# Kernel optimization log

Hardware: AMD Instinct MI355X
Metric: run time of the kernel (lower is better)

The kernel has to match this reference:

```python
import jax, jax.numpy as jnp
import numpy as np

HEADS = 4
DIM_HEAD = 64
SCALE = 8.0
EPS = 1e-5  # fp32 branch of the original LayerNorm


def setup_inputs() -> dict:
    key = jax.random.key(0)
    k1, k2, k3 = jax.random.split(key, 3)
    B, C, F, H, W = 2, 256, 4, 32, 32
    inner = HEADS * DIM_HEAD  # 256
    x = jax.random.normal(k1, (B, C, F, H, W), dtype=jnp.float32)
    gamma = jnp.ones((1, C, 1, 1, 1), dtype=jnp.float32)
    w_qkv = jax.random.normal(k2, (3 * inner, C), dtype=jnp.float32) * 0.05
    w_out = jax.random.normal(k3, (C, inner), dtype=jnp.float32) * 0.05
    return {"x": x, "gamma": gamma, "w_qkv": w_qkv, "w_out": w_out}


def _l2norm(t):
    return t / jnp.sqrt(jnp.sum(t * t, axis=-1, keepdims=True) + 1e-12)


def reference(x, gamma, w_qkv, w_out):
    B, C, F, H, W = x.shape
    N = F * H * W
    inner = HEADS * DIM_HEAD
    residual = x

    # channel LayerNorm (biased variance over dim=1)
    mean = jnp.mean(x, axis=1, keepdims=True)
    var = jnp.mean((x - mean) ** 2, axis=1, keepdims=True)
    xn = (x - mean) / jnp.sqrt(var + EPS) * gamma

    # 1x1x1 conv == channel matmul; flatten spatial dims to sequence
    xn_flat = xn.reshape(B, C, N)                      # [B, C, N]
    qkv = jnp.einsum('oc,bcn->bon', w_qkv, xn_flat)    # [B, 3*inner, N]
    qkv = qkv.reshape(B, 3, HEADS, DIM_HEAD, N)        # chunk then split heads
    qkv = jnp.transpose(qkv, (1, 0, 2, 4, 3))          # [3, B, h, N, d]
    q, k, v = qkv[0], qkv[1], qkv[2]

    q = _l2norm(q)
    k = _l2norm(k)

    sim = jnp.einsum('bhid,bhjd->bhij', q, k) * SCALE  # [B, h, N, N]
    attn = jax.nn.softmax(sim, axis=-1)
    out = jnp.einsum('bhij,bhjd->bhid', attn, v)       # [B, h, N, d]

    # 'b h n d -> b (h d) n' then 1x1x1 out conv
    out = jnp.transpose(out, (0, 1, 3, 2)).reshape(B, inner, N)
    out = jnp.einsum('oi,bin->bon', w_out, out).reshape(B, C, F, H, W)
    return out + residual
```

## Files before the change

kernel.cpp:

```cpp
#include <hip/hip_runtime.h>

#define BATCH 2
#define CCH   256
#define NSEQ  4096
#define NH    4
#define DH    64
#define INNER 256

typedef __attribute__((ext_vector_type(8))) __bf16 bf16x8;
typedef __attribute__((ext_vector_type(4))) float f32x4;
typedef __attribute__((ext_vector_type(8))) unsigned short u16x8;
typedef __attribute__((ext_vector_type(4))) unsigned short u16x4;

#define GLD16(gsrc, ldst)                                                     \
  __builtin_amdgcn_global_load_lds(                                           \
      (const __attribute__((address_space(1))) unsigned int*)(const void*)(gsrc), \
      (__attribute__((address_space(3))) unsigned int*)(void*)(ldst), 16, 0, 0)

static __device__ __forceinline__ unsigned short f2bfr(float f) {
  union { float f; unsigned u; } v; v.f = f;
  return (unsigned short)((v.u + 0x8000u) >> 16);
}
static __device__ __forceinline__ unsigned pack2(float f0, float f1) {
  union { float f; unsigned u; } a, b; a.f = f0; b.f = f1;
  return __builtin_amdgcn_perm(b.u + 0x8000u, a.u + 0x8000u, 0x07060302u);
}
static __device__ __forceinline__ float bf2f(unsigned short u) {
  union { unsigned u; float f; } v; v.u = ((unsigned)u) << 16;
  return v.f;
}
static __device__ __forceinline__ bf16x8 ldb(const unsigned short* p) {
  return *(const bf16x8*)p;
}
static __device__ __forceinline__ f32x4 mm(bf16x8 a, bf16x8 b, f32x4 c) {
  return __builtin_amdgcn_mfma_f32_16x16x32_bf16(a, b, c, 0, 0, 0);
}

__global__ __launch_bounds__(256) void k_lncvt(const float* __restrict__ x,
                                               const float* __restrict__ gamma,
                                               unsigned short* __restrict__ xn,
                                               const float* __restrict__ wq,
                                               const float* __restrict__ wo,
                                               unsigned short* __restrict__ wqb,
                                               unsigned short* __restrict__ wob) {
  int blk = blockIdx.x;
  if (blk >= 256) {
    int t = (blk - 256) * 256 + threadIdx.x;
    int e = t * 4;
    if (e < 768 * 256) {
      float4 v = *(const float4*)(wq + e);
      u16x4 pk = { f2bfr(v.x), f2bfr(v.y), f2bfr(v.z), f2bfr(v.w) };
      *(u16x4*)(wqb + e) = pk;
    } else {
      int e2 = e - 768 * 256;
      float4 v = *(const float4*)(wo + e2);
      u16x4 pk = { f2bfr(v.x), f2bfr(v.y), f2bfr(v.z), f2bfr(v.w) };
      *(u16x4*)(wob + e2) = pk;
    }
    return;
  }
  int b  = blk >> 7;
  int n0 = (blk & 127) * 32;
  int t  = threadIdx.x;
  int nl = t & 31;
  int cg = t >> 5;
  int n  = n0 + nl;
  const float* xp = x + ((size_t)(b * CCH + cg * 32)) * NSEQ + n;
  float vals[32];
  float s = 0.f, s2 = 0.f;
#pragma unroll
  for (int j = 0; j < 32; j++) {
    float v = xp[(size_t)j * NSEQ];
    vals[j] = v; s += v; s2 += v * v;
  }
  __shared__ float rs[8][32], rs2[8][32];
  rs[cg][nl] = s; rs2[cg][nl] = s2;
  __syncthreads();
  float S = 0.f, S2 = 0.f;
#pragma unroll
  for (int g = 0; g < 8; g++) { S += rs[g][nl]; S2 += rs2[g][nl]; }
  float mean = S * (1.f / 256.f);
  float var  = S2 * (1.f / 256.f) - mean * mean;
  float rstd = rsqrtf(var + 1e-5f);
  unsigned short* dst = xn + ((size_t)b * NSEQ + n) * CCH + cg * 32;
#pragma unroll
  for (int j0 = 0; j0 < 32; j0 += 8) {
    u16x8 pk;
#pragma unroll
    for (int j = 0; j < 8; j++)
      pk[j] = f2bfr((vals[j0 + j] - mean) * rstd * gamma[cg * 32 + j0 + j]);
    *(u16x8*)(dst + j0) = pk;
  }
}

__global__ __launch_bounds__(256) void k_qkv(const unsigned short* __restrict__ wqb,
                                             const unsigned short* __restrict__ xn,
                                             unsigned short* __restrict__ qkv,
                                             unsigned short* __restrict__ qt,
                                             unsigned short* __restrict__ ktb) {
  int n0 = blockIdx.x * 64;
  int oi = blockIdx.y;
  int o0 = oi * 64;
  int b  = blockIdx.z;
  __shared__ unsigned short Al[64 * 128];
  __shared__ unsigned short Bl[64 * 128];
  int t = threadIdx.x;
  int lane = t & 63, w = t >> 6;
  int c = lane & 15, quad = lane >> 4;
  int wm = w >> 1, wn = w & 1;
  f32x4 acc[2][2] = {};
  int lr = lane >> 4;
  int lchk = lane & 15;
  const unsigned short* apg = wqb + (size_t)o0 * CCH;
  const unsigned short* bpg = xn + ((size_t)b * NSEQ + n0) * CCH;
  for (int kt = 0; kt < 2; kt++) {
    if (kt) __syncthreads();
#pragma unroll
    for (int q = 0; q < 4; q++) {
      int r = w * 16 + q * 4 + lr;
      int srcoff = r * CCH + kt * 128 + ((lchk ^ (r & 7)) * 8);
      GLD16(apg + srcoff, Al + (size_t)(w * 16 + q * 4) * 128);
      GLD16(bpg + srcoff, Bl + (size_t)(w * 16 + q * 4) * 128);
    }
    __syncthreads();
#pragma unroll
    for (int ks = 0; ks < 4; ks++) {
      int ra0 = wm * 32 + c, ra1 = ra0 + 16;
      int rb0 = wn * 32 + c, rb1 = rb0 + 16;
      bf16x8 a0 = ldb(&Al[ra0 * 128 + (((ks * 4 + quad) ^ (ra0 & 7)) * 8)]);
      bf16x8 a1 = ldb(&Al[ra1 * 128 + (((ks * 4 + quad) ^ (ra1 & 7)) * 8)]);
      bf16x8 b0 = ldb(&Bl[rb0 * 128 + (((ks * 4 + quad) ^ (rb0 & 7)) * 8)]);
      bf16x8 b1 = ldb(&Bl[rb1 * 128 + (((ks * 4 + quad) ^ (rb1 & 7)) * 8)]);
      acc[0][0] = mm(a0, b0, acc[0][0]);
      acc[0][1] = mm(a0, b1, acc[0][1]);
      acc[1][0] = mm(a1, b0, acc[1][0]);
      acc[1][1] = mm(a1, b1, acc[1][1]);
    }
  }
  if (oi < 8) {
    float* sq = (float*)Al;
    float s0 = 0.f, s1 = 0.f;
#pragma unroll
    for (int i = 0; i < 2; i++)
#pragma unroll
      for (int rr = 0; rr < 4; rr++) {
        s0 += acc[i][0][rr] * acc[i][0][rr];
        s1 += acc[i][1][rr] * acc[i][1][rr];
      }
    s0 += __shfl_xor(s0, 16); s0 += __shfl_xor(s0, 32);
    s1 += __shfl_xor(s1, 16); s1 += __shfl_xor(s1, 32);
    __syncthreads();
    if (quad == 0) {
      sq[wm * 64 + wn * 32 + c]      = s0;
      sq[wm * 64 + wn * 32 + 16 + c] = s1;
    }
    __syncthreads();
    float r0 = rsqrtf(sq[wn * 32 + c]      + sq[64 + wn * 32 + c]      + 1e-12f);
    float r1 = rsqrtf(sq[wn * 32 + 16 + c] + sq[64 + wn * 32 + 16 + c] + 1e-12f);
    if (oi < 4) { r0 *= 11.541560327111707f; r1 *= 11.541560327111707f; }
    int h = oi & 3;
    unsigned short* base = (oi < 4 ? qt : ktb) + ((size_t)(b * NH + h) * NSEQ) * DH;
#pragma unroll
    for (int i = 0; i < 2; i++)
#pragma unroll
      for (int j = 0; j < 2; j++) {
        float rsc = j ? r1 : r0;
        int n = n0 + wn * 32 + j * 16 + c;
        int d = wm * 32 + i * 16 + quad * 4;
        uint2 pk = { pack2(acc[i][j][0] * rsc, acc[i][j][1] * rsc),
                     pack2(acc[i][j][2] * rsc, acc[i][j][3] * rsc) };
        *(uint2*)(base + (size_t)n * DH + d) = pk;
      }
  } else {
#pragma unroll
    for (int i = 0; i < 2; i++)
#pragma unroll
      for (int j = 0; j < 2; j++)
#pragma unroll
        for (int rr = 0; rr < 4; rr++) {
          int o = o0 + wm * 32 + i * 16 + quad * 4 + rr;
          int n = n0 + wn * 32 + j * 16 + c;
          qkv[((size_t)b * 768 + o) * NSEQ + n] = f2bfr(acc[i][j][rr]);
        }
  }
}

__global__ __launch_bounds__(256, 4) void k_attn(
    const unsigned short* __restrict__ qt,
    const unsigned short* __restrict__ ktb,
    const unsigned short* __restrict__ qkv,
    unsigned short* __restrict__ opart,
    float* __restrict__ lpart,
    int S, int kvlen) {
  int i0 = blockIdx.x * 128;
  int h  = blockIdx.y;
  int bz = blockIdx.z;
  int b  = bz / S, s = bz % S;
  __shared__ unsigned short Kl[64 * 64];
  __shared__ unsigned short Vl[64 * 64];
  __shared__ unsigned short Pl[128 * 64];
  int t = threadIdx.x;
  int lane = t & 63, w = t >> 6;
  int c = lane & 15, quad = lane >> 4;

  const unsigned short* qbase = qt  + ((size_t)(b * NH + h) * NSEQ) * DH;
  const unsigned short* kbase = ktb + ((size_t)(b * NH + h) * NSEQ) * DH;
  const unsigned short* vbase = qkv + ((size_t)b * 768 + 512 + h * 64) * NSEQ;

  int rlo = w * 32 + c, rhi = rlo + 16;
  const unsigned short* qlo = qbase + (size_t)(i0 + rlo) * DH + quad * 8;
  const unsigned short* qhi = qlo + 16 * DH;
  bf16x8 qlo0 = ldb(qlo), qlo1 = ldb(qlo + 32);
  bf16x8 qhi0 = ldb(qhi), qhi1 = ldb(qhi + 32);

  u16x8 onesu;
#pragma unroll
  for (int j = 0; j < 8; j++) onesu[j] = 0x3F80;
  bf16x8 ones = *(bf16x8*)&onesu;

  f32x4 acclo[4] = {}, acchi[4] = {};
  f32x4 accllo = {}, acclhi = {};

  int slr = lane >> 3, slc = lane & 7;
  int ssw = (slc ^ slr) * 8;
  const unsigned short* kp = kbase + (size_t)(s * kvlen + w * 16 + slr) * DH + ssw;
  const unsigned short* vp = vbase + (size_t)(w * 16 + slr) * NSEQ + s * kvlen + ssw;
  unsigned short* kl0 = Kl + (w * 16)     * 64;
  unsigned short* kl1 = Kl + (w * 16 + 8) * 64;
  unsigned short* vl0 = Vl + (w * 16)     * 64;
  unsigned short* vl1 = Vl + (w * 16 + 8) * 64;
  int sw0 = (quad ^ (c & 7)) * 8;
  int sw1 = sw0 ^ 32;
  int r7 = rlo & 7;

  for (int it = 0; it < kvlen / 64; it++) {
    GLD16(kp,            kl0);
    GLD16(kp + 8 * DH,   kl1);
    GLD16(vp,            vl0);
    GLD16(vp + 8 * NSEQ, vl1);
    kp += 64 * DH; vp += 64;
    __syncthreads();

#pragma unroll
    for (int jt = 0; jt < 4; jt++) {
      bf16x8 k0 = ldb(&Kl[(jt * 16 + c) * 64 + sw0]);
      bf16x8 k1 = ldb(&Kl[(jt * 16 + c) * 64 + sw1]);
      f32x4 zl = {}; zl = mm(k0, qlo0, zl); zl = mm(k1, qlo1, zl);
      f32x4 zh = {}; zh = mm(k0, qhi0, zh); zh = mm(k1, qhi1, zh);
      int cj = jt * 2 + (quad >> 1);
      int sub = (quad & 1) * 4;
      uint2 pkl = { pack2(exp2f(zl[0]), exp2f(zl[1])),
                    pack2(exp2f(zl[2]), exp2f(zl[3])) };
      *(uint2*)&Pl[rlo * 64 + ((cj ^ r7) * 8) + sub] = pkl;
      uint2 pkh = { pack2(exp2f(zh[0]), exp2f(zh[1])),
                    pack2(exp2f(zh[2]), exp2f(zh[3])) };
      *(uint2*)&Pl[rhi * 64 + ((cj ^ r7) * 8) + sub] = pkh;
    }
    bf16x8 plo0 = ldb(&Pl[rlo * 64 + ((quad ^ r7) * 8)]);
    bf16x8 plo1 = ldb(&Pl[rlo * 64 + (((quad + 4) ^ r7) * 8)]);
    bf16x8 phi0 = ldb(&Pl[rhi * 64 + ((quad ^ r7) * 8)]);
    bf16x8 phi1 = ldb(&Pl[rhi * 64 + (((quad + 4) ^ r7) * 8)]);
#pragma unroll
    for (int dt = 0; dt < 4; dt++) {
      bf16x8 v0 = ldb(&Vl[(dt * 16 + c) * 64 + sw0]);
      bf16x8 v1 = ldb(&Vl[(dt * 16 + c) * 64 + sw1]);
      acclo[dt] = mm(plo0, v0, acclo[dt]);
      acclo[dt] = mm(plo1, v1, acclo[dt]);
      acchi[dt] = mm(phi0, v0, acchi[dt]);
      acchi[dt] = mm(phi1, v1, acchi[dt]);
    }
    accllo = mm(plo0, ones, accllo); accllo = mm(plo1, ones, accllo);
    acclhi = mm(phi0, ones, acclhi); acclhi = mm(phi1, ones, acclhi);
    __syncthreads();
  }

  size_t rb = ((size_t)(b * NH + h) * S + s) * NSEQ + i0 + w * 32;
  if (c == 0) {
#pragma unroll
    for (int rr = 0; rr < 4; rr++) {
      lpart[rb + quad * 4 + rr]      = accllo[rr];
      lpart[rb + 16 + quad * 4 + rr] = acclhi[rr];
    }
  }
#pragma unroll
  for (int rr = 0; rr < 4; rr++)
#pragma unroll
    for (int dt = 0; dt < 4; dt++) {
      opart[(rb + quad * 4 + rr) * 64 + dt * 16 + c]      = f2bfr(acclo[dt][rr]);
      opart[(rb + 16 + quad * 4 + rr) * 64 + dt * 16 + c] = f2bfr(acchi[dt][rr]);
    }
}

__global__ __launch_bounds__(256) void k_out(const unsigned short* __restrict__ wob,
                                             const unsigned short* __restrict__ opart,
                                             const float* __restrict__ lpart,
                                             const float* __restrict__ x,
                                             float* __restrict__ out, int S) {
  int n0 = blockIdx.x * 64;
  int o0 = blockIdx.y * 64;
  int b  = blockIdx.z;
  __shared__ unsigned short Al[64 * 128];
  __shared__ unsigned short Bl[64 * 128];
  int t = threadIdx.x;
  int lane = t & 63, w = t >> 6;
  int c = lane & 15, quad = lane >> 4;
  int wm = w >> 1, wn = w & 1;
  f32x4 acc[2][2] = {};
  int lr = lane >> 4;
  int lchk = lane & 15;
  const unsigned short* apg = wob + (size_t)o0 * INNER;
  int br = t >> 2;
  int n  = n0 + br;
  for (int kt = 0; kt < 2; kt++) {
    if (kt) __syncthreads();
#pragma unroll
    for (int q = 0; q < 4; q++) {
      int r = w * 16 + q * 4 + lr;
      int srcoff = r * INNER + kt * 128 + ((lchk ^ (r & 7)) * 8);
      GLD16(apg + srcoff, Al + (size_t)(w * 16 + q * 4) * 128);
    }
    float linv[2];
#pragma unroll
    for (int hh = 0; hh < 2; hh++) {
      int h = kt * 2 + hh;
      float l = 0.f;
      for (int s = 0; s < S; s++)
        l += lpart[((size_t)(b * NH + h) * S + s) * NSEQ + n];
      linv[hh] = 1.f / l;
    }
#pragma unroll
    for (int q = 0; q < 4; q++) {
      int cj = (t & 3) + 4 * q;
      int hh = cj >> 3;
      int h  = kt * 2 + hh;
      int d  = (cj & 7) * 8;
      float o[8] = {};
      for (int s = 0; s < S; s++) {
        const unsigned short* p =
            opart + (((size_t)(b * NH + h) * S + s) * NSEQ + n) * 64 + d;
        u16x8 v = *(const u16x8*)p;
#pragma unroll
        for (int j = 0; j < 8; j++) o[j] += bf2f(v[j]);
      }
      float iv = linv[hh];
      uint4 pk = { pack2(o[0] * iv, o[1] * iv), pack2(o[2] * iv, o[3] * iv),
                   pack2(o[4] * iv, o[5] * iv), pack2(o[6] * iv, o[7] * iv) };
      *(uint4*)&Bl[br * 128 + ((cj ^ (br & 7)) * 8)] = pk;
    }
    __syncthreads();
#pragma unroll
    for (int ks = 0; ks < 4; ks++) {
      int ra0 = wm * 32 + c, ra1 = ra0 + 16;
      int rb0 = wn * 32 + c, rb1 = rb0 + 16;
      bf16x8 a0 = ldb(&Al[ra0 * 128 + (((ks * 4 + quad) ^ (ra0 & 7)) * 8)]);
      bf16x8 a1 = ldb(&Al[ra1 * 128 + (((ks * 4 + quad) ^ (ra1 & 7)) * 8)]);
      bf16x8 b0 = ldb(&Bl[rb0 * 128 + (((ks * 4 + quad) ^ (rb0 & 7)) * 8)]);
      bf16x8 b1 = ldb(&Bl[rb1 * 128 + (((ks * 4 + quad) ^ (rb1 & 7)) * 8)]);
      acc[0][0] = mm(a0, b0, acc[0][0]);
      acc[0][1] = mm(a0, b1, acc[0][1]);
      acc[1][0] = mm(a1, b0, acc[1][0]);
      acc[1][1] = mm(a1, b1, acc[1][1]);
    }
  }
#pragma unroll
  for (int i = 0; i < 2; i++)
#pragma unroll
    for (int j = 0; j < 2; j++)
#pragma unroll
      for (int rr = 0; rr < 4; rr++) {
        int o = o0 + wm * 32 + i * 16 + quad * 4 + rr;
        int nn = n0 + wn * 32 + j * 16 + c;
        size_t idx = ((size_t)b * CCH + o) * NSEQ + nn;
        out[idx] = acc[i][j][rr] + x[idx];
      }
}

extern "C" void kernel_launch(void* const* d_in, const int* in_sizes, int n_in,
                              void* d_out, int out_size, void* d_ws, size_t ws_size,
                              hipStream_t stream) {
  const float* x     = (const float*)d_in[0];
  const float* gamma = (const float*)d_in[1];
  const float* wq    = (const float*)d_in[2];
  const float* wo    = (const float*)d_in[3];
  float* out = (float*)d_out;

  const size_t MB = 1u << 20;
  char* ws = (char*)d_ws;
  unsigned short* xn  = (unsigned short*)ws;
  unsigned short* qkv = (unsigned short*)(ws + 4 * MB);
  unsigned short* wqb = (unsigned short*)(ws + 16 * MB);
  unsigned short* wob = (unsigned short*)(ws + 16 * MB + 512 * 1024);
  unsigned short* qt  = (unsigned short*)(ws + 17 * MB);
  unsigned short* ktb = (unsigned short*)(ws + 21 * MB);
  unsigned short* opart = (unsigned short*)(ws + 25 * MB);
  int S;
  if (ws_size >= 45 * MB) S = 4;
  else if (ws_size >= 36 * MB) S = 2;
  else S = 1;
  size_t opart_bytes = (size_t)S * BATCH * NH * NSEQ * DH * 2;
  float* lpart = (float*)(ws + 25 * MB + opart_bytes);
  int kvlen = NSEQ / S;

  k_lncvt<<<dim3(512),          256, 0, stream>>>(x, gamma, xn, wq, wo, wqb, wob);
  k_qkv  <<<dim3(64, 12, 2),    256, 0, stream>>>(wqb, xn, qkv, qt, ktb);
  k_attn <<<dim3(32, 4, 2 * S), 256, 0, stream>>>(qt, ktb, qkv, opart,
                                                  lpart, S, kvlen);
  k_out  <<<dim3(64, 4, 2),     256, 0, stream>>>(wob, opart, lpart, x, out, S);
}
```

Measured before the change: 148.6 us.

## Double-buffer K/V tiles in attention and split partial merge into its own kernel

```diff
diff --git a/kernel.cpp b/kernel.cpp
--- a/kernel.cpp
+++ b/kernel.cpp
@@ -185,7 +185,7 @@
   }
 }
 
-__global__ __launch_bounds__(256, 4) void k_attn(
+__global__ __launch_bounds__(256, 3) void k_attn(
     const unsigned short* __restrict__ qt,
     const unsigned short* __restrict__ ktb,
     const unsigned short* __restrict__ qkv,
@@ -196,8 +196,8 @@
   int h  = blockIdx.y;
   int bz = blockIdx.z;
   int b  = bz / S, s = bz % S;
-  __shared__ unsigned short Kl[64 * 64];
-  __shared__ unsigned short Vl[64 * 64];
+  __shared__ unsigned short Kl[2][64 * 64];
+  __shared__ unsigned short Vl[2][64 * 64];
   __shared__ unsigned short Pl[128 * 64];
   int t = threadIdx.x;
   int lane = t & 63, w = t >> 6;
@@ -225,26 +225,33 @@
   int ssw = (slc ^ slr) * 8;
   const unsigned short* kp = kbase + (size_t)(s * kvlen + w * 16 + slr) * DH + ssw;
   const unsigned short* vp = vbase + (size_t)(w * 16 + slr) * NSEQ + s * kvlen + ssw;
-  unsigned short* kl0 = Kl + (w * 16)     * 64;
-  unsigned short* kl1 = Kl + (w * 16 + 8) * 64;
-  unsigned short* vl0 = Vl + (w * 16)     * 64;
-  unsigned short* vl1 = Vl + (w * 16 + 8) * 64;
   int sw0 = (quad ^ (c & 7)) * 8;
   int sw1 = sw0 ^ 32;
   int r7 = rlo & 7;
 
-  for (int it = 0; it < kvlen / 64; it++) {
-    GLD16(kp,            kl0);
-    GLD16(kp + 8 * DH,   kl1);
-    GLD16(vp,            vl0);
-    GLD16(vp + 8 * NSEQ, vl1);
-    kp += 64 * DH; vp += 64;
+  int nIt = kvlen / 64;
+  GLD16(kp,            &Kl[0][(w * 16)     * 64]);
+  GLD16(kp + 8 * DH,   &Kl[0][(w * 16 + 8) * 64]);
+  GLD16(vp,            &Vl[0][(w * 16)     * 64]);
+  GLD16(vp + 8 * NSEQ, &Vl[0][(w * 16 + 8) * 64]);
+  kp += 64 * DH; vp += 64;
+
+  for (int it = 0; it < nIt; it++) {
+    int cur = it & 1;
     __syncthreads();
+    if (it + 1 < nIt) {
+      int nb = cur ^ 1;
+      GLD16(kp,            &Kl[nb][(w * 16)     * 64]);
+      GLD16(kp + 8 * DH,   &Kl[nb][(w * 16 + 8) * 64]);
+      GLD16(vp,            &Vl[nb][(w * 16)     * 64]);
+      GLD16(vp + 8 * NSEQ, &Vl[nb][(w * 16 + 8) * 64]);
+      kp += 64 * DH; vp += 64;
+    }
 
 #pragma unroll
     for (int jt = 0; jt < 4; jt++) {
-      bf16x8 k0 = ldb(&Kl[(jt * 16 + c) * 64 + sw0]);
-      bf16x8 k1 = ldb(&Kl[(jt * 16 + c) * 64 + sw1]);
+      bf16x8 k0 = ldb(&Kl[cur][(jt * 16 + c) * 64 + sw0]);
+      bf16x8 k1 = ldb(&Kl[cur][(jt * 16 + c) * 64 + sw1]);
       f32x4 zl = {}; zl = mm(k0, qlo0, zl); zl = mm(k1, qlo1, zl);
       f32x4 zh = {}; zh = mm(k0, qhi0, zh); zh = mm(k1, qhi1, zh);
       int cj = jt * 2 + (quad >> 1);
@@ -262,8 +269,8 @@
     bf16x8 phi1 = ldb(&Pl[rhi * 64 + (((quad + 4) ^ r7) * 8)]);
 #pragma unroll
     for (int dt = 0; dt < 4; dt++) {
-      bf16x8 v0 = ldb(&Vl[(dt * 16 + c) * 64 + sw0]);
-      bf16x8 v1 = ldb(&Vl[(dt * 16 + c) * 64 + sw1]);
+      bf16x8 v0 = ldb(&Vl[cur][(dt * 16 + c) * 64 + sw0]);
+      bf16x8 v1 = ldb(&Vl[cur][(dt * 16 + c) * 64 + sw1]);
       acclo[dt] = mm(plo0, v0, acclo[dt]);
       acclo[dt] = mm(plo1, v1, acclo[dt]);
       acchi[dt] = mm(phi0, v0, acchi[dt]);
@@ -271,7 +278,6 @@
     }
     accllo = mm(plo0, ones, accllo); accllo = mm(plo1, ones, accllo);
     acclhi = mm(phi0, ones, acclhi); acclhi = mm(phi1, ones, acclhi);
-    __syncthreads();
   }
 
   size_t rb = ((size_t)(b * NH + h) * S + s) * NSEQ + i0 + w * 32;
@@ -291,11 +297,46 @@
     }
 }
 
+__global__ __launch_bounds__(256) void k_merge(
+    const unsigned short* __restrict__ opart,
+    const float* __restrict__ lpart,
+    unsigned short* __restrict__ ao, int S) {
+  int t = blockIdx.x * 256 + threadIdx.x;
+  int row = t >> 2;
+  int dseg = (t & 3) * 16;
+  int b = row >> 14, rem = row & 16383;
+  int h = rem >> 12, i = rem & 4095;
+
+  float l = 0.f;
+  float o[16];
+#pragma unroll
+  for (int j = 0; j < 16; j++) o[j] = 0.f;
+  for (int s = 0; s < S; s++) {
+    size_t rb = ((size_t)(b * NH + h) * S + s) * NSEQ + i;
+    l += lpart[rb];
+    const unsigned short* p = opart + rb * 64 + dseg;
+    u16x8 v0 = *(const u16x8*)p;
+    u16x8 v1 = *(const u16x8*)(p + 8);
+#pragma unroll
+    for (int j = 0; j < 8; j++) {
+      o[j]     += bf2f(v0[j]);
+      o[8 + j] += bf2f(v1[j]);
+    }
+  }
+  float inv = 1.f / l;
+  unsigned short* dst = ao + ((size_t)b * NSEQ + i) * INNER + h * 64 + dseg;
+  uint4 pk0 = { pack2(o[0] * inv, o[1] * inv),  pack2(o[2] * inv, o[3] * inv),
+                pack2(o[4] * inv, o[5] * inv),  pack2(o[6] * inv, o[7] * inv) };
+  uint4 pk1 = { pack2(o[8] * inv, o[9] * inv),  pack2(o[10] * inv, o[11] * inv),
+                pack2(o[12] * inv, o[13] * inv),pack2(o[14] * inv, o[15] * inv) };
+  *(uint4*)dst = pk0;
+  *(uint4*)(dst + 8) = pk1;
+}
+
 __global__ __launch_bounds__(256) void k_out(const unsigned short* __restrict__ wob,
-                                             const unsigned short* __restrict__ opart,
-                                             const float* __restrict__ lpart,
+                                             const unsigned short* __restrict__ ao,
                                              const float* __restrict__ x,
-                                             float* __restrict__ out, int S) {
+                                             float* __restrict__ out) {
   int n0 = blockIdx.x * 64;
   int o0 = blockIdx.y * 64;
   int b  = blockIdx.z;
@@ -309,8 +350,7 @@
   int lr = lane >> 4;
   int lchk = lane & 15;
   const unsigned short* apg = wob + (size_t)o0 * INNER;
-  int br = t >> 2;
-  int n  = n0 + br;
+  const unsigned short* bpg = ao + ((size_t)b * NSEQ + n0) * INNER;
   for (int kt = 0; kt < 2; kt++) {
     if (kt) __syncthreads();
 #pragma unroll
@@ -318,34 +358,7 @@
       int r = w * 16 + q * 4 + lr;
       int srcoff = r * INNER + kt * 128 + ((lchk ^ (r & 7)) * 8);
       GLD16(apg + srcoff, Al + (size_t)(w * 16 + q * 4) * 128);
-    }
-    float linv[2];
-#pragma unroll
-    for (int hh = 0; hh < 2; hh++) {
-      int h = kt * 2 + hh;
-      float l = 0.f;
-      for (int s = 0; s < S; s++)
-        l += lpart[((size_t)(b * NH + h) * S + s) * NSEQ + n];
-      linv[hh] = 1.f / l;
-    }
-#pragma unroll
-    for (int q = 0; q < 4; q++) {
-      int cj = (t & 3) + 4 * q;
-      int hh = cj >> 3;
-      int h  = kt * 2 + hh;
-      int d  = (cj & 7) * 8;
-      float o[8] = {};
-      for (int s = 0; s < S; s++) {
-        const unsigned short* p =
-            opart + (((size_t)(b * NH + h) * S + s) * NSEQ + n) * 64 + d;
-        u16x8 v = *(const u16x8*)p;
-#pragma unroll
-        for (int j = 0; j < 8; j++) o[j] += bf2f(v[j]);
-      }
-      float iv = linv[hh];
-      uint4 pk = { pack2(o[0] * iv, o[1] * iv), pack2(o[2] * iv, o[3] * iv),
-                   pack2(o[4] * iv, o[5] * iv), pack2(o[6] * iv, o[7] * iv) };
-      *(uint4*)&Bl[br * 128 + ((cj ^ (br & 7)) * 8)] = pk;
+      GLD16(bpg + srcoff, Bl + (size_t)(w * 16 + q * 4) * 128);
     }
     __syncthreads();
 #pragma unroll
@@ -369,8 +382,8 @@
 #pragma unroll
       for (int rr = 0; rr < 4; rr++) {
         int o = o0 + wm * 32 + i * 16 + quad * 4 + rr;
-        int nn = n0 + wn * 32 + j * 16 + c;
-        size_t idx = ((size_t)b * CCH + o) * NSEQ + nn;
+        int n = n0 + wn * 32 + j * 16 + c;
+        size_t idx = ((size_t)b * CCH + o) * NSEQ + n;
         out[idx] = acc[i][j][rr] + x[idx];
       }
 }
@@ -386,24 +399,26 @@
 
   const size_t MB = 1u << 20;
   char* ws = (char*)d_ws;
-  unsigned short* xn  = (unsigned short*)ws;
-  unsigned short* qkv = (unsigned short*)(ws + 4 * MB);
-  unsigned short* wqb = (unsigned short*)(ws + 16 * MB);
-  unsigned short* wob = (unsigned short*)(ws + 16 * MB + 512 * 1024);
-  unsigned short* qt  = (unsigned short*)(ws + 17 * MB);
-  unsigned short* ktb = (unsigned short*)(ws + 21 * MB);
-  unsigned short* opart = (unsigned short*)(ws + 25 * MB);
+  unsigned short* ao  = (unsigned short*)ws;
+  unsigned short* xn  = (unsigned short*)(ws + 4 * MB);
+  unsigned short* qkv = (unsigned short*)(ws + 8 * MB);
+  unsigned short* wqb = (unsigned short*)(ws + 20 * MB);
+  unsigned short* wob = (unsigned short*)(ws + 20 * MB + 512 * 1024);
+  unsigned short* qt  = (unsigned short*)(ws + 21 * MB);
+  unsigned short* ktb = (unsigned short*)(ws + 25 * MB);
+  unsigned short* opart = (unsigned short*)(ws + 29 * MB);
   int S;
-  if (ws_size >= 45 * MB) S = 4;
-  else if (ws_size >= 36 * MB) S = 2;
+  if (ws_size >= 48 * MB) S = 4;
+  else if (ws_size >= 40 * MB) S = 2;
   else S = 1;
   size_t opart_bytes = (size_t)S * BATCH * NH * NSEQ * DH * 2;
-  float* lpart = (float*)(ws + 25 * MB + opart_bytes);
+  float* lpart = (float*)(ws + 29 * MB + opart_bytes);
   int kvlen = NSEQ / S;
 
   k_lncvt<<<dim3(512),          256, 0, stream>>>(x, gamma, xn, wq, wo, wqb, wob);
   k_qkv  <<<dim3(64, 12, 2),    256, 0, stream>>>(wqb, xn, qkv, qt, ktb);
   k_attn <<<dim3(32, 4, 2 * S), 256, 0, stream>>>(qt, ktb, qkv, opart,
                                                   lpart, S, kvlen);
-  k_out  <<<dim3(64, 4, 2),     256, 0, stream>>>(wob, opart, lpart, x, out, S);
-}
+  k_merge<<<dim3(512),          256, 0, stream>>>(opart, lpart, ao, S);
+  k_out  <<<dim3(64, 4, 2),     256, 0, stream>>>(wob, ao, x, out);
+}
```

After: 145.5 us. 2.1% less time.
